# Kernel tuning notes

Measured on AMD Instinct MI355X. Metric: run time of the kernel, lower is better.

Reference implementation:

```python
import jax, jax.numpy as jnp
import numpy as np

Nh = 128
B = 4096


def _conv3d(x, w):
    # x: [B, C, D, H, W], w: [O, I, 3, 3, 3], same padding, no bias
    return jax.lax.conv_general_dilated(
        x, w, window_strides=(1, 1, 1), padding=[(1, 1)] * 3,
        dimension_numbers=("NCDHW", "OIDHW", "NCDHW"))


def setup_inputs() -> dict:
    key = jax.random.key(0)
    ks = jax.random.split(key, 12)
    x = jax.random.normal(ks[0], (B, 1024), dtype=jnp.float32)
    hidden_states = jax.random.normal(ks[1], (B, Nh, 4, 4, 4), dtype=jnp.float32)
    cw = 0.05  # small init for conv kernels
    Wz = jax.random.normal(ks[2], (Nh, Nh, 3, 3, 3), dtype=jnp.float32) * cw
    Wr = jax.random.normal(ks[3], (Nh, Nh, 3, 3, 3), dtype=jnp.float32) * cw
    Wm = jax.random.normal(ks[4], (Nh, Nh, 3, 3, 3), dtype=jnp.float32) * cw
    # biases init like np.random.rand -> uniform [0,1)
    bz = jax.random.uniform(ks[5], (1, Nh, 4, 4, 4), dtype=jnp.float32)
    br = jax.random.uniform(ks[6], (1, Nh, 4, 4, 4), dtype=jnp.float32)
    bm = jax.random.uniform(ks[7], (1, Nh, 4, 4, 4), dtype=jnp.float32)
    lw = 0.03
    Lz = jax.random.normal(ks[8], (Nh * 64, 1024), dtype=jnp.float32) * lw
    Lr = jax.random.normal(ks[9], (Nh * 64, 1024), dtype=jnp.float32) * lw
    Lm = jax.random.normal(ks[10], (Nh * 64, 1024), dtype=jnp.float32) * lw
    return dict(x=x, hidden_states=hidden_states, Wz=Wz, Wr=Wr, Wm=Wm,
                bz=bz, br=br, bm=bm, Lz=Lz, Lr=Lr, Lm=Lm)


def reference(x, hidden_states, Wz, Wr, Wm, bz, br, bm, Lz, Lr, Lm):
    # linear projections (torch Linear: x @ W.T), reshaped to voxel grid
    lz = (x @ Lz.T).reshape(B, Nh, 4, 4, 4)
    lr = (x @ Lr.T).reshape(B, Nh, 4, 4, 4)
    lm = (x @ Lm.T).reshape(B, Nh, 4, 4, 4)
    z = jax.nn.sigmoid(_conv3d(hidden_states, Wz) + lz + bz)
    r = jax.nn.sigmoid(_conv3d(hidden_states, Wr) + lr + br)
    mem = jnp.tanh(_conv3d(r * hidden_states, Wm) + lm + bm)
    return (1.0 - z) * hidden_states + z * mem
```

## Files before the change

kernel.cpp:

```cpp
#include <hip/hip_runtime.h>
#include <cstdint>

typedef __attribute__((ext_vector_type(8))) short bf16x8;
typedef __attribute__((ext_vector_type(4))) float f32x4;
typedef unsigned short u16;
typedef unsigned int u32;

static const size_t OFF_WT = 0;
static const size_t OFF_XB = 2654464;
static const size_t OFF_LB = 11043072;
static const size_t OFF_HT = 61374720;
static const size_t OFF_RH = 128483584;

__device__ __forceinline__ u16 f2bf(float x) {
  union { float f; u32 u; } v; v.f = x;
  u32 r = (v.u + 0x7FFFu + ((v.u >> 16) & 1u)) >> 16;
  return (u16)r;
}
__device__ __forceinline__ float bf2f(u16 x) {
  union { u32 u; float f; } v; v.u = ((u32)x) << 16; return v.f;
}

__device__ __forceinline__ void gload16(const void* g, void* l) {
  __builtin_amdgcn_global_load_lds(
      (const __attribute__((address_space(1))) uint32_t*)g,
      (__attribute__((address_space(3))) uint32_t*)l, 16, 0, 0);
}

__global__ __launch_bounds__(256) void k_cvt(
    const float* __restrict__ x,
    const float* __restrict__ Wz, const float* __restrict__ Wr, const float* __restrict__ Wm,
    const float* __restrict__ Lz, const float* __restrict__ Lr, const float* __restrict__ Lm,
    uint8_t* __restrict__ ws) {
  u16* wt = (u16*)(ws + OFF_WT);
  u16* xb = (u16*)(ws + OFF_XB);
  u16* lb = (u16*)(ws + OFF_LB);
  const long NWT = 3L * 27 * 128 * 128;
  const long NX  = 4096L * 1024;
  const long NL  = 3L * 8192 * 1024;
  const long total = NWT + NX + NL;
  for (long i = (long)blockIdx.x * blockDim.x + threadIdx.x; i < total;
       i += (long)gridDim.x * blockDim.x) {
    if (i < NWT) {
      long g = i / (27L * 16384);
      long r = i % (27L * 16384);
      long t = r / 16384;
      long oc = (r / 128) % 128;
      long ic = r % 128;
      const float* W = (g == 0) ? Wz : ((g == 1) ? Wr : Wm);
      wt[i] = f2bf(W[(oc * 128 + ic) * 27 + t]);
    } else if (i < NWT + NX) {
      long j = i - NWT;
      xb[j] = f2bf(x[j]);
    } else {
      long j = i - NWT - NX;
      long g = j / (8192L * 1024);
      long r = j % (8192L * 1024);
      const float* L = (g == 0) ? Lz : ((g == 1) ? Lr : Lm);
      lb[j] = f2bf(L[r]);
    }
  }
}

__global__ __launch_bounds__(256) void k_ht(const float* __restrict__ h, uint8_t* __restrict__ ws) {
  __shared__ float tile[128 * 65];
  int b = blockIdx.x;
  const float* hb = h + (size_t)b * 8192;
  u16* ht = (u16*)(ws + OFF_HT) + (size_t)b * 8192;
  for (int i = threadIdx.x; i < 8192; i += 256) {
    int ic = i >> 6, vo = i & 63;
    tile[ic * 65 + vo] = hb[i];
  }
  __syncthreads();
  for (int i = threadIdx.x; i < 8192; i += 256) {
    int vo = i >> 7, ic = i & 127;
    ht[i] = f2bf(tile[ic * 65 + vo]);
  }
}

template <int MODE>
__global__ __launch_bounds__(256) void k_conv_gemm(
    uint8_t* __restrict__ ws,
    const float* __restrict__ bz, const float* __restrict__ br, const float* __restrict__ bm,
    u32* __restrict__ dout) {
  int bx = blockIdx.x;
  int g, vo, mb;
  if (MODE == 0) {
    int L = (bx & 7) * 512 + (bx >> 3);
    g = L & 1; vo = (L >> 1) & 63; mb = L >> 7;
  } else {
    int L = (bx & 7) * 256 + (bx >> 3);
    g = 2; vo = L & 63; mb = L >> 6;
  }

  const uint8_t* wt_b = ws + OFF_WT + (size_t)g * 27 * 32768;
  const uint8_t* xb_b = ws + OFF_XB;
  const uint8_t* lb_b = ws + OFF_LB + (size_t)g * 8192 * 2048;
  const uint8_t* as_b = ws + ((MODE == 0) ? OFF_HT : OFF_RH);

  __shared__ __align__(1024) uint8_t lds[65536];

  const int tid = threadIdx.x;
  const int w = tid >> 6;
  const int l = tid & 63;
  const int lrow = l >> 3;
  const int co = (((l & 7) ^ lrow) << 4);
  const int wm = (w >> 1) * 64;
  const int wn = (w & 1) * 64;
  const int lr16 = l & 15;
  const int lk = l >> 4;

  f32x4 acc[4][4];
#pragma unroll
  for (int m = 0; m < 4; ++m)
#pragma unroll
    for (int n = 0; n < 4; ++n) acc[m][n] = (f32x4){0.f, 0.f, 0.f, 0.f};

  const uint8_t* aA_x = xb_b + ((size_t)(mb * 128 + w * 32 + lrow)) * 2048 + co;
  const uint8_t* aA_t = as_b + ((size_t)(mb * 128 + w * 32 + lrow)) * 16384 + co;
  const uint8_t* aB_x = lb_b + ((size_t)(w * 32 + lrow)) * 131072 + (size_t)vo * 2048 + co;
  const uint8_t* aB_t = wt_b + ((size_t)(w * 32 + lrow)) * 256 + co;

  const int d = vo >> 4, e = (vo >> 2) & 3, f = vo & 3;
  auto validT = [&](int t) {
    int p3 = t / 9 - 1, q3 = (t / 3) % 3 - 1, s3 = t % 3 - 1;
    int dd = d + p3, ee = e + q3, ff = f + s3;
    return dd >= 0 && dd <= 3 && ee >= 0 && ee <= 3 && ff >= 0 && ff <= 3;
  };
  const int nd = 3 - (d == 0) - (d == 3);
  const int ne = 3 - (e == 0) - (e == 3);
  const int nf = 3 - (f == 0) - (f == 3);
  const int NP = 16 + 2 * nd * ne * nf;

  int s_kt = 0;
  int s_t = 0, s_ih = 0;
  while (!validT(s_t)) ++s_t;

  auto stage_next = [&](int buf) {
    uint8_t* Ad = lds + buf * 32768 + w * 4096;
    uint8_t* Bd = lds + buf * 32768 + 16384 + w * 4096;
    if (s_kt < 16) {
      int kt = s_kt;
#pragma unroll
      for (int pp = 0; pp < 4; ++pp)
        gload16(aA_x + (size_t)kt * 128 + pp * 16384, Ad + pp * 1024);
#pragma unroll
      for (int pp = 0; pp < 4; ++pp)
        gload16(aB_x + (size_t)kt * 128 + (size_t)pp * 1048576, Bd + pp * 1024);
      ++s_kt;
    } else {
      int t = s_t, ih = s_ih;
      int dd = d + t / 9 - 1, ee = e + (t / 3) % 3 - 1, ff = f + t % 3 - 1;
      int vi = dd * 16 + ee * 4 + ff;
#pragma unroll
      for (int pp = 0; pp < 4; ++pp)
        gload16(aA_t + (size_t)vi * 256 + ih * 128 + pp * 131072, Ad + pp * 1024);
#pragma unroll
      for (int pp = 0; pp < 4; ++pp)
        gload16(aB_t + (size_t)t * 32768 + ih * 128 + pp * 2048, Bd + pp * 1024);
      s_ih ^= 1;
      if (!s_ih) { do { ++s_t; } while (s_t < 27 && !validT(s_t)); }
    }
  };

  auto compute = [&](int buf) {
    const u16* At = (const u16*)(lds + buf * 32768);
    const u16* Bt = (const u16*)(lds + buf * 32768 + 16384);
#pragma unroll
    for (int ks = 0; ks < 2; ++ks) {
      bf16x8 af[4], bfr[4];
#pragma unroll
      for (int m = 0; m < 4; ++m) {
        int row = wm + m * 16 + lr16;
        int c = ks * 4 + lk;
        af[m] = *(const bf16x8*)&At[row * 64 + ((c ^ (row & 7)) * 8)];
      }
#pragma unroll
      for (int n = 0; n < 4; ++n) {
        int row = wn + n * 16 + lr16;
        int c = ks * 4 + lk;
        bfr[n] = *(const bf16x8*)&Bt[row * 64 + ((c ^ (row & 7)) * 8)];
      }
#pragma unroll
      for (int m = 0; m < 4; ++m)
#pragma unroll
        for (int n = 0; n < 4; ++n)
          acc[m][n] = __builtin_amdgcn_mfma_f32_16x16x32_bf16(af[m], bfr[n], acc[m][n], 0, 0, 0);
    }
  };

  stage_next(0);
  __syncthreads();
  for (int p = 0; p < NP; ++p) {
    int cur = p & 1;
    if (p + 1 < NP) stage_next(cur ^ 1);
    compute(cur);
    __syncthreads();
  }

  const float* bias = (MODE == 0) ? ((g == 0) ? bz : br) : bm;
  const u16* htp = (const u16*)(ws + OFF_HT);
  u16* rhp = (u16*)(ws + OFF_RH);
#pragma unroll
  for (int n = 0; n < 4; ++n) {
    int oc = wn + n * 16 + lr16;
    float bv = bias[oc * 64 + vo];
#pragma unroll
    for (int m = 0; m < 4; ++m) {
#pragma unroll
      for (int j = 0; j < 4; ++j) {
        int brow = mb * 128 + wm + m * 16 + lk * 4 + j;
        size_t pidx = (size_t)brow * 8192 + (size_t)vo * 128 + oc;
        float pre = acc[m][n][j] + bv;
        pre = fminf(fmaxf(pre, -30.f), 30.f);
        if (MODE == 0) {
          float sg = 1.f / (1.f + __expf(-pre));
          if (g == 0) {
            dout[pidx] = (u32)f2bf(sg);
          } else {
            float hv = bf2f(htp[pidx]);
            rhp[pidx] = f2bf(sg * hv);
          }
        } else {
          float e2 = __expf(-2.f * pre);
          float th = (1.f - e2) / (1.f + e2);
          u32 old = dout[pidx];
          dout[pidx] = (old & 0xFFFFu) | (((u32)f2bf(th)) << 16);
        }
      }
    }
  }
}

__global__ __launch_bounds__(256) void k_combine(const float* __restrict__ h, u32* __restrict__ dout) {
  __shared__ u32 tile[64 * 129];
  int b = blockIdx.x;
  const u32* db = dout + (size_t)b * 8192;
  for (int i = threadIdx.x; i < 8192; i += 256) {
    int vo = i >> 7, oc = i & 127;
    tile[vo * 129 + oc] = db[i];
  }
  __syncthreads();
  float* ob = (float*)dout + (size_t)b * 8192;
  const float* hb = h + (size_t)b * 8192;
  for (int o = threadIdx.x; o < 8192; o += 256) {
    int oc = o >> 6, vo = o & 63;
    u32 pk = tile[vo * 129 + oc];
    float z = bf2f((u16)(pk & 0xFFFFu));
    float mem = bf2f((u16)(pk >> 16));
    ob[o] = (1.f - z) * hb[o] + z * mem;
  }
}

extern "C" void kernel_launch(void* const* d_in, const int* in_sizes, int n_in,
                              void* d_out, int out_size, void* d_ws, size_t ws_size,
                              hipStream_t stream) {
  const float* x  = (const float*)d_in[0];
  const float* h  = (const float*)d_in[1];
  const float* Wz = (const float*)d_in[2];
  const float* Wr = (const float*)d_in[3];
  const float* Wm = (const float*)d_in[4];
  const float* bz = (const float*)d_in[5];
  const float* br = (const float*)d_in[6];
  const float* bm = (const float*)d_in[7];
  const float* Lz = (const float*)d_in[8];
  const float* Lr = (const float*)d_in[9];
  const float* Lm = (const float*)d_in[10];
  uint8_t* ws = (uint8_t*)d_ws;
  u32* dout = (u32*)d_out;

  k_cvt<<<2048, 256, 0, stream>>>(x, Wz, Wr, Wm, Lz, Lr, Lm, ws);
  k_ht<<<4096, 256, 0, stream>>>(h, ws);
  k_conv_gemm<0><<<4096, 256, 0, stream>>>(ws, bz, br, bm, dout);
  k_conv_gemm<1><<<2048, 256, 0, stream>>>(ws, bz, br, bm, dout);
  k_combine<<<4096, 256, 0, stream>>>(h, dout);
}
```

Before: 935.4 us.

## Single-buffer A tile and preload fragments to cut LDS for higher occupancy

Cuts the conv-GEMM kernel's LDS from 64KB to 48KB by keeping a single A buffer and double-buffering only B, and sets launch bounds to target 3 blocks per CU. To make the single A buffer safe, each iteration first loads all A/B fragments into registers, then synchronizes, then issues the next stage's loads before running the MFMAs. This adds an extra barrier per iteration and raises register pressure under the tighter launch bound, which may cause spills. In exchange it aims for more resident blocks to hide global-load latency.

Measured after the change: 879.2 us, median of 2. -6.0%, faster.

```diff
diff --git a/kernel.cpp b/kernel.cpp
--- a/kernel.cpp
+++ b/kernel.cpp
@@ -79,7 +79,7 @@
 }
 
 template <int MODE>
-__global__ __launch_bounds__(256) void k_conv_gemm(
+__global__ __launch_bounds__(256, 3) void k_conv_gemm(
     uint8_t* __restrict__ ws,
     const float* __restrict__ bz, const float* __restrict__ br, const float* __restrict__ bm,
     u32* __restrict__ dout) {
@@ -98,7 +98,7 @@
   const uint8_t* lb_b = ws + OFF_LB + (size_t)g * 8192 * 2048;
   const uint8_t* as_b = ws + ((MODE == 0) ? OFF_HT : OFF_RH);
 
-  __shared__ __align__(1024) uint8_t lds[65536];
+  __shared__ __align__(1024) uint8_t lds[49152];
 
   const int tid = threadIdx.x;
   const int w = tid >> 6;
@@ -136,9 +136,9 @@
   int s_t = 0, s_ih = 0;
   while (!validT(s_t)) ++s_t;
 
-  auto stage_next = [&](int buf) {
-    uint8_t* Ad = lds + buf * 32768 + w * 4096;
-    uint8_t* Bd = lds + buf * 32768 + 16384 + w * 4096;
+  auto stage_next = [&](int bbuf) {
+    uint8_t* Ad = lds + w * 4096;
+    uint8_t* Bd = lds + 16384 + bbuf * 16384 + w * 4096;
     if (s_kt < 16) {
       int kt = s_kt;
 #pragma unroll
@@ -163,38 +163,38 @@
     }
   };
 
-  auto compute = [&](int buf) {
-    const u16* At = (const u16*)(lds + buf * 32768);
-    const u16* Bt = (const u16*)(lds + buf * 32768 + 16384);
-#pragma unroll
-    for (int ks = 0; ks < 2; ++ks) {
-      bf16x8 af[4], bfr[4];
-#pragma unroll
-      for (int m = 0; m < 4; ++m) {
-        int row = wm + m * 16 + lr16;
-        int c = ks * 4 + lk;
-        af[m] = *(const bf16x8*)&At[row * 64 + ((c ^ (row & 7)) * 8)];
-      }
-#pragma unroll
-      for (int n = 0; n < 4; ++n) {
-        int row = wn + n * 16 + lr16;
-        int c = ks * 4 + lk;
-        bfr[n] = *(const bf16x8*)&Bt[row * 64 + ((c ^ (row & 7)) * 8)];
-      }
-#pragma unroll
-      for (int m = 0; m < 4; ++m)
-#pragma unroll
-        for (int n = 0; n < 4; ++n)
-          acc[m][n] = __builtin_amdgcn_mfma_f32_16x16x32_bf16(af[m], bfr[n], acc[m][n], 0, 0, 0);
-    }
-  };
-
   stage_next(0);
   __syncthreads();
   for (int p = 0; p < NP; ++p) {
     int cur = p & 1;
+    const u16* At = (const u16*)lds;
+    const u16* Bt = (const u16*)(lds + 16384 + cur * 16384);
+    bf16x8 af[4][2], bfr[4][2];
+#pragma unroll
+    for (int m = 0; m < 4; ++m)
+#pragma unroll
+      for (int ks = 0; ks < 2; ++ks) {
+        int row = wm + m * 16 + lr16;
+        int c = ks * 4 + lk;
+        af[m][ks] = *(const bf16x8*)&At[row * 64 + ((c ^ (row & 7)) * 8)];
+      }
+#pragma unroll
+    for (int n = 0; n < 4; ++n)
+#pragma unroll
+      for (int ks = 0; ks < 2; ++ks) {
+        int row = wn + n * 16 + lr16;
+        int c = ks * 4 + lk;
+        bfr[n][ks] = *(const bf16x8*)&Bt[row * 64 + ((c ^ (row & 7)) * 8)];
+      }
+    __syncthreads();
     if (p + 1 < NP) stage_next(cur ^ 1);
-    compute(cur);
+#pragma unroll
+    for (int ks = 0; ks < 2; ++ks)
+#pragma unroll
+      for (int m = 0; m < 4; ++m)
+#pragma unroll
+        for (int n = 0; n < 4; ++n)
+          acc[m][n] = __builtin_amdgcn_mfma_f32_16x16x32_bf16(af[m][ks], bfr[n][ks], acc[m][n], 0, 0, 0);
     __syncthreads();
   }
 
```
